# Optimization experiments

Measured on AMD Instinct MI355X. Metric: run time of the kernel, lower is better.

## Reference

```python
import jax, jax.numpy as jnp
import numpy as np

B, T, D, K, DEPTH = 8, 1024, 128, 64, 1


def _rel_ids(T, k):
    # relative_mat_id[i, j] = clamp(k + j - i, 0, 2k)
    base = jnp.arange(k, k + T)[None, :] - jnp.arange(T)[:, None]
    return jnp.clip(base, 0, 2 * k)  # [T, T] int32


def setup_inputs() -> dict:
    key = jax.random.key(0)
    ks = jax.random.split(key, 13)
    s = 1.0 / np.sqrt(D)
    return {
        "x": jax.random.normal(ks[0], (B, T, D), dtype=jnp.float32),
        "W0": jax.random.normal(ks[1], (D, D), dtype=jnp.float32) * s,
        "b0": jnp.zeros((D,), dtype=jnp.float32),
        "Wq": jax.random.normal(ks[2], (D, D), dtype=jnp.float32) * s,
        "bq": jnp.zeros((D,), dtype=jnp.float32),
        "Wk": jax.random.normal(ks[3], (D, D), dtype=jnp.float32) * s,
        "bk": jnp.zeros((D,), dtype=jnp.float32),
        "Wv": jax.random.normal(ks[4], (D, D), dtype=jnp.float32) * s,
        "bv": jnp.zeros((D,), dtype=jnp.float32),
        "W1": jax.random.normal(ks[5], (D, D), dtype=jnp.float32) * s,
        "b1": jnp.zeros((D,), dtype=jnp.float32),
        "pe_key": jax.random.normal(ks[6], (2 * K + 1, D), dtype=jnp.float32) * np.sqrt(2.0 / (2 * K + 1)),
        "pe_value": jax.random.normal(ks[7], (2 * K + 1, D), dtype=jnp.float32) * np.sqrt(2.0 / (2 * K + 1)),
    }


def reference(x, W0, b0, Wq, bq, Wk, bk, Wv, bv, W1, b1, pe_key, pe_value):
    Tlen = x.shape[1]
    ids = _rel_ids(Tlen, K)                     # [T, T]
    rpr_key = pe_key[ids]                       # [T, T, D]
    rpr_value = pe_value[ids]                   # [T, T, D]

    hs = jax.nn.relu(x @ W0 + b0)               # fc0 (dropout = eval identity)
    for _ in range(DEPTH):
        q = jnp.tanh(hs @ Wq + bq)
        k = jnp.tanh(hs @ Wk + bk)
        v = jnp.tanh(hs @ Wv + bv)
        a = jnp.einsum("bid,bjd->bij", q, k)
        a = a + jnp.einsum("ijd,bid->bij", rpr_key, q)
        a = jax.nn.softmax(a, axis=2)
        c = jnp.einsum("bij,bjd->bid", a, v)
        c = c + jnp.einsum("bij,ijd->bid", a, rpr_value)
        hs = jax.nn.relu(c @ W1 + b1)
    return hs
```

## Files before the change

kernel.cpp:

```cpp
#include <hip/hip_runtime.h>


#define TT 1024
#define DD 128
#define NB 8
#define SJH 1160

typedef _Float16 f16;
typedef __attribute__((ext_vector_type(8))) _Float16 f16x8;
typedef __attribute__((ext_vector_type(4))) _Float16 f16x4;
typedef __attribute__((ext_vector_type(4))) float f32x4;

static __device__ inline float fast_tanh(float x) {
    float xc = fminf(fmaxf(x, -12.f), 12.f);
    float e = __expf(2.f * xc);
    return (e - 1.f) / (e + 1.f);
}

#define GLDS(gp, lp) __builtin_amdgcn_global_load_lds( \
    (const __attribute__((address_space(1))) unsigned*)(gp), \
    (__attribute__((address_space(3))) unsigned*)(lp), 16, 0, 0)

__global__ __launch_bounds__(256) void prep_all(
        const float* __restrict__ W0, const float* __restrict__ Wq,
        const float* __restrict__ Wk, const float* __restrict__ Wv,
        const float* __restrict__ W1, const float* __restrict__ PEK,
        const float* __restrict__ PEV, char* __restrict__ wimg,
        char* __restrict__ pekimg, char* __restrict__ pevimg) {
    const int blk = blockIdx.x, t = threadIdx.x;
    if (blk < 5) {
        const float* W = blk == 0 ? W0 : blk == 1 ? Wq : blk == 2 ? Wk
                       : blk == 3 ? Wv : W1;
        char* o = wimg + (size_t)blk * 32768;
        #pragma unroll
        for (int it = 0; it < 8; it++) {
            int item = t + 256 * it;
            int n = item & 127, k0 = (item >> 7) * 8;
            f16x8 h;
            #pragma unroll
            for (int e = 0; e < 8; e++) h[e] = (f16)W[(k0 + e) * 128 + n];
            *(f16x8*)(o + n * 256 + ((2 * k0) ^ ((n & 7) << 4))) = h;
        }
    } else if (blk == 5) {
        for (int it = 0; it < 64; it++) {
            int idx = t + 256 * it;
            int m = idx >> 7, d = idx & 127;
            *(f16*)(pekimg + (m >> 6) * 16384 + (m & 63) * 256
                    + ((2 * d) ^ ((m & 7) << 4))) = (f16)PEK[m * 128 + d];
        }
    } else {
        for (int it = 0; it < 64; it++) {
            int idx = t + 256 * it;
            int m = idx >> 7, d = idx & 127;
            *(f16*)(pevimg + (m >> 5) * 8192 + d * 64
                    + ((2 * (m & 31)) ^ ((d & 3) << 4))) = (f16)PEV[m * 128 + d];
        }
    }
}

#define ZACC() do { _Pragma("unroll") for (int _i = 0; _i < 2; _i++) \
    _Pragma("unroll") for (int _j = 0; _j < 2; _j++) \
        acc[_i][_j] = (f32x4){0.f, 0.f, 0.f, 0.f}; } while (0)

#define GEMMCORE(SRC, WL) do { \
    _Pragma("unroll") for (int _c = 0; _c < 4; _c++) { \
        f16x8 _af[2], _bf[2]; \
        _Pragma("unroll") for (int _it = 0; _it < 2; _it++) { \
            int _row = _it * 16 + (l & 15); \
            int _a = (_row << 8) + (_c << 6) + ((l >> 4) << 4); \
            _af[_it] = *(const f16x8*)((SRC) + (_a ^ ((_row & 7) << 4))); } \
        _Pragma("unroll") for (int _nt = 0; _nt < 2; _nt++) { \
            int _n = wv * 32 + _nt * 16 + (l & 15); \
            int _a = (_n << 8) + (_c << 6) + ((l >> 4) << 4); \
            _bf[_nt] = *(const f16x8*)((WL) + (_a ^ ((_n & 7) << 4))); } \
        _Pragma("unroll") for (int _it = 0; _it < 2; _it++) \
        _Pragma("unroll") for (int _nt = 0; _nt < 2; _nt++) \
            acc[_it][_nt] = __builtin_amdgcn_mfma_f32_16x16x32_f16( \
                    _af[_it], _bf[_nt], acc[_it][_nt], 0, 0, 0); } } while (0)

#define ISSUEW(wi, dst) do { \
    const char* _g = wimg + (size_t)(wi) * 32768 + t * 16; \
    char* _d = (dst) + t * 16; \
    _Pragma("unroll") for (int _i = 0; _i < 8; _i++) \
        GLDS(_g + _i * 4096, _d + _i * 4096); \
} while (0)

#define WAITBAR(N) do { \
    asm volatile("s_waitcnt vmcnt(" #N ") lgkmcnt(0)" ::: "memory"); \
    __builtin_amdgcn_s_barrier(); \
    __builtin_amdgcn_sched_barrier(0); \
} while (0)

__global__ __launch_bounds__(256) void fused_qkv(
        const float* __restrict__ x, const char* __restrict__ wimg,
        const float* __restrict__ b0, const float* __restrict__ bq,
        const float* __restrict__ bk, const float* __restrict__ bv,
        f16* __restrict__ q16, char* __restrict__ kimg,
        char* __restrict__ vimg) {
    extern __shared__ __align__(16) char smq[];
    char* xs  = smq;
    char* hsl = smq + 8192;
    char* wA  = smq + 16384;
    char* wB  = smq + 49152;
    char* wC  = smq + 81920;
    const int t = threadIdx.x, wv = t >> 6, l = t & 63;
    const int blk = blockIdx.x;

    const int r0 = (blk & 7) * 1024 + (blk >> 3) * 32;
    ISSUEW(0, wA);
    ISSUEW(1, wB);
    {
        const float* X = x + (size_t)r0 * 128;
        #pragma unroll
        for (int i = 0; i < 2; i++) {
            f32x4 a0 = *(const f32x4*)(X + t * 16 + i * 8);
            f32x4 a1 = *(const f32x4*)(X + t * 16 + i * 8 + 4);
            f16x8 h;
            h[0]=(f16)a0[0]; h[1]=(f16)a0[1]; h[2]=(f16)a0[2]; h[3]=(f16)a0[3];
            h[4]=(f16)a1[0]; h[5]=(f16)a1[1]; h[6]=(f16)a1[2]; h[7]=(f16)a1[3];
            int a = t * 32 + i * 16;
            *(f16x8*)(xs + (a ^ (((a >> 8) & 7) << 4))) = h;
        }
    }
    WAITBAR(8);

    f32x4 acc[2][2];
    ZACC();
    GEMMCORE(xs, wA);
    {
        #pragma unroll
        for (int it = 0; it < 2; it++)
            #pragma unroll
            for (int nt = 0; nt < 2; nt++) {
                int n = wv * 32 + nt * 16 + (l & 15);
                float bb = b0[n];
                #pragma unroll
                for (int r = 0; r < 4; r++) {
                    int i = it * 16 + (l >> 4) * 4 + r;
                    float v = fmaxf(acc[it][nt][r] + bb, 0.f);
                    int a = i * 256 + 2 * n;
                    *(f16*)(hsl + (a ^ ((i & 7) << 4))) = (f16)v;
                }
            }
    }
    ISSUEW(2, wC);
    WAITBAR(8);

    ZACC();
    GEMMCORE(hsl, wB);
    {
        #pragma unroll
        for (int it = 0; it < 2; it++)
            #pragma unroll
            for (int nt = 0; nt < 2; nt++) {
                int n = wv * 32 + nt * 16 + (l & 15);
                float bb = bq[n];
                #pragma unroll
                for (int r = 0; r < 4; r++) {
                    int i = it * 16 + (l >> 4) * 4 + r;
                    q16[(size_t)(r0 + i) * 128 + n] =
                            (f16)fast_tanh(acc[it][nt][r] + bb);
                }
            }
    }
    ISSUEW(3, wA);
    WAITBAR(8);

    ZACC();
    GEMMCORE(hsl, wC);
    f16* ts = (f16*)xs;
    {
        #pragma unroll
        for (int it = 0; it < 2; it++)
            #pragma unroll
            for (int nt = 0; nt < 2; nt++) {
                int n = wv * 32 + nt * 16 + (l & 15);
                float bb = bk[n];
                #pragma unroll
                for (int r = 0; r < 4; r++) {
                    int i = it * 16 + (l >> 4) * 4 + r;
                    ts[i * 128 + n] = (f16)fast_tanh(acc[it][nt][r] + bb);
                }
            }
    }
    WAITBAR(0);

    {
        #pragma unroll
        for (int half = 0; half < 2; half++) {
            int row = (t >> 4) + half * 16;
            int seg = t & 15;
            int jg = r0 + row;
            int chunk = ((jg >> 10) << 4) + ((jg & 1023) >> 6);
            int jp = jg & 63;
            char* dst = kimg + (size_t)chunk * 16384 + jp * 256
                      + ((seg * 16) ^ ((jp & 7) << 4));
            *(f16x8*)dst = *(const f16x8*)&ts[row * 128 + seg * 8];
        }
    }
    ZACC();
    GEMMCORE(hsl, wA);
    {
        #pragma unroll
        for (int it = 0; it < 2; it++)
            #pragma unroll
            for (int nt = 0; nt < 2; nt++) {
                int d = wv * 32 + nt * 16 + (l & 15);
                float bb = bv[d];
                f16x4 h;
                #pragma unroll
                for (int r = 0; r < 4; r++)
                    h[r] = (f16)fast_tanh(acc[it][nt][r] + bb);
                int jb = r0 + it * 16 + ((l >> 4) << 2);
                int chunk = ((jb >> 10) << 5) + ((jb & 1023) >> 5);
                char* dst = vimg + (size_t)chunk * 8192 + d * 64
                          + ((2 * (jb & 31)) ^ ((d & 3) << 4));
                *(f16x4*)dst = h;
            }
    }
}

#define ISSUE16(src, bi) do { const char* _g = (src) + t * 16; \
    char* _d = BUF + (size_t)(bi) * 16384 + t * 16; \
    GLDS(_g, _d); GLDS(_g + 4096, _d + 4096); \
    GLDS(_g + 8192, _d + 8192); GLDS(_g + 12288, _d + 12288); \
} while (0)

#define ISSUE8(src, s8) do { const char* _g = (src) + t * 16; \
    char* _d = BUF + (size_t)(s8) * 8192 + t * 16; \
    GLDS(_g, _d); GLDS(_g + 4096, _d + 4096); \
} while (0)

__global__ __launch_bounds__(256) void attn_all(
        const f16* __restrict__ q16, const char* __restrict__ kimg,
        const char* __restrict__ pekimg, const char* __restrict__ vimg,
        const char* __restrict__ pevimg, const float* __restrict__ PEK,
        const float* __restrict__ PEV, const char* __restrict__ w1img,
        const float* __restrict__ b1, float* __restrict__ out) {
    extern __shared__ __align__(16) char sm7[];
    f16*   S   = (f16*)sm7;
    char*  BUF = sm7 + 37120;
    f16*   QB  = (f16*)(sm7 + 69888);
    float* LR  = (float*)(sm7 + 74112);

    const int t = threadIdx.x, wv = t >> 6, l = t & 63;
    const int lr = l & 15, lg = l >> 4;
    const int b = blockIdx.x & 7;
    const int i0 = (blockIdx.x >> 3) << 4;

    f16x8 qf[4];
    {
        const f16* qb = q16 + (size_t)(b * TT + i0 + lr) * 128 + lg * 8;
        #pragma unroll
        for (int c = 0; c < 4; c++) qf[c] = *(const f16x8*)(qb + c * 32);
    }
    const int row2 = t >> 4, l16 = t & 15;
    f16x8 qpv = *(const f16x8*)(q16 + (size_t)(b * TT + i0 + row2) * 128 + l16 * 8);
    f32x4 pkv0 = *(const f32x4*)(PEK + 128 * 128 + l16 * 8);
    f32x4 pkv1 = *(const f32x4*)(PEK + 128 * 128 + l16 * 8 + 4);
    f32x4 pvr4[2];
    #pragma unroll
    for (int dt = 0; dt < 2; dt++)
        pvr4[dt] = *(const f32x4*)(PEV + 128 * 128 + wv * 32 + dt * 16 + lg * 4);
    float bb1[2];
    #pragma unroll
    for (int nt = 0; nt < 2; nt++) bb1[nt] = b1[wv * 32 + nt * 16 + lr];

    const char* kbase = kimg + (size_t)b * 16 * 16384;
    const char* vbase = vimg + (size_t)b * 32 * 8192;

    ISSUE16(kbase, 0);

    for (int ch = 0; ch < 18; ch++) {
        asm volatile("s_waitcnt vmcnt(0)" ::: "memory");
        __builtin_amdgcn_s_barrier();
        __builtin_amdgcn_sched_barrier(0);
        {
            int ci = ch + 1;
            if (ci < 16)      ISSUE16(kbase + (size_t)ci * 16384, ci & 1);
            else if (ci < 18) ISSUE16(pekimg + (size_t)(ci - 16) * 16384, ci & 1);
            else {
                ISSUE8(vbase, 0);
                ISSUE8(vbase + 8192, 1);
            }
        }
        const char* kb = BUF + (size_t)(ch & 1) * 16384;
        const int jp = wv * 16 + lr;
        f32x4 a2 = {0.f, 0.f, 0.f, 0.f};
        #pragma unroll
        for (int c = 0; c < 4; c++) {
            f16x8 kf = *(const f16x8*)(kb + jp * 256
                        + ((c * 64 + lg * 16) ^ ((jp & 7) << 4)));
            a2 = __builtin_amdgcn_mfma_f32_16x16x32_f16(kf, qf[c], a2, 0, 0, 0);
        }
        f16x4 h = {(f16)a2[0], (f16)a2[1], (f16)a2[2], (f16)a2[3]};
        *(f16x4*)&S[lr * SJH + ch * 64 + wv * 16 + lg * 4] = h;
    }
    asm volatile("s_waitcnt lgkmcnt(0)" ::: "memory");
    __builtin_amdgcn_s_barrier();
    __builtin_amdgcn_sched_barrier(0);

    {
        const int ig = i0 + row2;
        f16* srow = S + row2 * SJH;
        f16* qrow = QB + row2 * 132;

        float qp;
        {
            float s = 0.f;
            #pragma unroll
            for (int e = 0; e < 4; e++) s += (float)qpv[e] * pkv0[e];
            #pragma unroll
            for (int e = 0; e < 4; e++) s += (float)qpv[e + 4] * pkv1[e];
            #pragma unroll
            for (int off = 8; off; off >>= 1) s += __shfl_xor(s, off, 64);
            qp = s;
        }
        for (int mm = l16; mm < 128; mm += 16) {
            qrow[mm] = srow[1024 + mm];
            srow[1024 + mm] = (f16)0.f;
        }
        if (l16 == 0) qrow[128] = (f16)qp;
        const float qlo = (float)qrow[0], qhi = qp;

        float lmax = -3.0e38f;
        #pragma unroll
        for (int kk = 0; kk < 8; kk++) {
            int j0 = kk * 128 + l16 * 8;
            f16x8 sv = *(const f16x8*)(srow + j0);
            #pragma unroll
            for (int e = 0; e < 8; e++) {
                int idd = 64 + j0 + e - ig;
                float qv = (idd <= 0) ? qlo : (idd >= 128 ? qhi : (float)qrow[idd]);
                lmax = fmaxf(lmax, (float)sv[e] + qv);
            }
        }
        #pragma unroll
        for (int off = 8; off; off >>= 1) lmax = fmaxf(lmax, __shfl_xor(lmax, off, 64));

        float lsum = 0.f, s0 = 0.f, s1 = 0.f;
        #pragma unroll
        for (int kk = 0; kk < 8; kk++) {
            int j0 = kk * 128 + l16 * 8;
            f16x8 sv = *(const f16x8*)(srow + j0);
            f16x8 pv;
            #pragma unroll
            for (int e = 0; e < 8; e++) {
                int idd = 64 + j0 + e - ig;
                float qv = (idd <= 0) ? qlo : (idd >= 128 ? qhi : (float)qrow[idd]);
                float p = __expf((float)sv[e] + qv - lmax);
                pv[e] = (f16)p;
                lsum += p;
                if (idd <= 0)        s0 += p;
                else if (idd >= 128) s1 += p;
                else                 srow[1024 + idd] = (f16)p;
            }
            *(f16x8*)(srow + j0) = pv;
        }
        #pragma unroll
        for (int off = 8; off; off >>= 1) {
            lsum += __shfl_xor(lsum, off, 64);
            s0   += __shfl_xor(s0,   off, 64);
            s1   += __shfl_xor(s1,   off, 64);
        }
        if (l16 == 0) {
            srow[1024] = (f16)s0;
            srow[1152] = (f16)s1;
            LR[row2] = lsum;
        }
    }
    asm volatile("s_waitcnt lgkmcnt(0)" ::: "memory");
    __builtin_amdgcn_s_barrier();
    __builtin_amdgcn_sched_barrier(0);
    ISSUE8(vbase + 2 * 8192, 2);

    f32x4 cacc[2] = {};
    for (int ch = 0; ch < 36; ch++) {
        asm volatile("s_waitcnt vmcnt(4)" ::: "memory");
        __builtin_amdgcn_s_barrier();
        __builtin_amdgcn_sched_barrier(0);
        {
            int ci = ch + 3;
            if (ci < 32)      ISSUE8(vbase + (size_t)ci * 8192, ci & 3);
            else if (ci < 36) ISSUE8(pevimg + (size_t)(ci - 32) * 8192, ci & 3);
            else              ISSUE8(w1img + (size_t)(ci - 36) * 8192, ci & 3);
        }
        const char* vb = BUF + (size_t)(ch & 3) * 8192;
        f16x8 pf = *(const f16x8*)&S[lr * SJH + ch * 32 + lg * 8];
        #pragma unroll
        for (int dt = 0; dt < 2; dt++) {
            int dp = wv * 32 + dt * 16 + lr;
            f16x8 vf = *(const f16x8*)(vb + dp * 64
                        + ((lg * 16) ^ ((dp & 3) << 4)));
            cacc[dt] = __builtin_amdgcn_mfma_f32_16x16x32_f16(vf, pf, cacc[dt], 0, 0, 0);
        }
    }

    const float w128 = (float)S[lr * SJH + 1152];
    const float rden = 1.f / LR[lr];
    asm volatile("s_waitcnt lgkmcnt(0)" ::: "memory");
    __builtin_amdgcn_s_barrier();
    __builtin_amdgcn_sched_barrier(0);
    ISSUE8(w1img + 3 * 8192, 3);
    char* cl = (char*)S;
    #pragma unroll
    for (int dt = 0; dt < 2; dt++) {
        #pragma unroll
        for (int r = 0; r < 4; r++) {
            int d = wv * 32 + dt * 16 + lg * 4 + r;
            float cv = (cacc[dt][r] + w128 * pvr4[dt][r]) * rden;
            int a = lr * 256 + 2 * d;
            *(f16*)(cl + (a ^ ((lr & 7) << 4))) = (f16)cv;
        }
    }
    asm volatile("s_waitcnt vmcnt(0) lgkmcnt(0)" ::: "memory");
    __builtin_amdgcn_s_barrier();
    __builtin_amdgcn_sched_barrier(0);

    const char* wl4 = BUF;
    f32x4 oacc[2] = {};
    #pragma unroll
    for (int c = 0; c < 4; c++) {
        int aa = lr * 256 + c * 64 + lg * 16;
        f16x8 af = *(const f16x8*)(cl + (aa ^ ((lr & 7) << 4)));
        #pragma unroll
        for (int nt = 0; nt < 2; nt++) {
            int n = wv * 32 + nt * 16 + lr;
            int ba = n * 256 + c * 64 + lg * 16;
            f16x8 bf = *(const f16x8*)(wl4 + (ba ^ ((n & 7) << 4)));
            oacc[nt] = __builtin_amdgcn_mfma_f32_16x16x32_f16(af, bf, oacc[nt], 0, 0, 0);
        }
    }
    #pragma unroll
    for (int nt = 0; nt < 2; nt++) {
        int n = wv * 32 + nt * 16 + lr;
        #pragma unroll
        for (int r = 0; r < 4; r++) {
            int i = lg * 4 + r;
            out[(size_t)(b * TT + i0 + i) * DD + n] = fmaxf(oacc[nt][r] + bb1[nt], 0.f);
        }
    }
}


extern "C" void kernel_launch(void* const* d_in, const int* in_sizes, int n_in,
                              void* d_out, int out_size, void* d_ws, size_t ws_size,
                              hipStream_t stream) {
    const float* x   = (const float*)d_in[0];
    const float* W0  = (const float*)d_in[1];
    const float* b0  = (const float*)d_in[2];
    const float* Wq  = (const float*)d_in[3];
    const float* bq  = (const float*)d_in[4];
    const float* Wk  = (const float*)d_in[5];
    const float* bk  = (const float*)d_in[6];
    const float* Wv  = (const float*)d_in[7];
    const float* bv  = (const float*)d_in[8];
    const float* W1  = (const float*)d_in[9];
    const float* b1  = (const float*)d_in[10];
    const float* pek = (const float*)d_in[11];
    const float* pev = (const float*)d_in[12];
    float* out = (float*)d_out;

    const size_t NTD = (size_t)NB * TT * DD;
    f16* q16     = (f16*)d_ws;
    char* wimg   = (char*)(q16 + NTD);
    char* kimg   = wimg + 5 * 32768;
    char* vimg   = kimg + (size_t)128 * 16384;
    char* pekimg = vimg + (size_t)256 * 8192;
    char* pevimg = pekimg + 32768;

    const int SMEM_QKV  = 114688;
    const int SMEM_ATTN = 74176;
    hipFuncSetAttribute(reinterpret_cast<const void*>(fused_qkv),
                        hipFuncAttributeMaxDynamicSharedMemorySize, SMEM_QKV);
    hipFuncSetAttribute(reinterpret_cast<const void*>(attn_all),
                        hipFuncAttributeMaxDynamicSharedMemorySize, SMEM_ATTN);

    hipLaunchKernelGGL(prep_all, dim3(7), dim3(256), 0, stream,
                       W0, Wq, Wk, Wv, W1, pek, pev, wimg, pekimg, pevimg);
    hipLaunchKernelGGL(fused_qkv, dim3(256), dim3(256), SMEM_QKV, stream,
                       x, wimg, b0, bq, bk, bv, q16, kimg, vimg);
    hipLaunchKernelGGL(attn_all, dim3(512), dim3(256), SMEM_ATTN, stream,
                       q16, kimg, pekimg, vimg, pevimg, pek, pev,
                       wimg + 4 * 32768, b1, out);
}
```

Measured before the change: 51.06 us.

## Split attention over key halves with a separate softmax combine kernel

Result: slower. 60.66 us (+18.8%).

```diff
diff --git a/kernel.cpp b/kernel.cpp
--- a/kernel.cpp
+++ b/kernel.cpp
@@ -4,7 +4,7 @@
 #define TT 1024
 #define DD 128
 #define NB 8
-#define SJH 1160
+#define SW 648
 
 typedef _Float16 f16;
 typedef __attribute__((ext_vector_type(8))) _Float16 f16x8;
@@ -26,7 +26,7 @@
         const float* __restrict__ Wk, const float* __restrict__ Wv,
         const float* __restrict__ W1, const float* __restrict__ PEK,
         const float* __restrict__ PEV, char* __restrict__ wimg,
-        char* __restrict__ pekimg, char* __restrict__ pevimg) {
+        char* __restrict__ pek4, char* __restrict__ pevt) {
     const int blk = blockIdx.x, t = threadIdx.x;
     if (blk < 5) {
         const float* W = blk == 0 ? W0 : blk == 1 ? Wq : blk == 2 ? Wk
@@ -45,15 +45,16 @@
         for (int it = 0; it < 64; it++) {
             int idx = t + 256 * it;
             int m = idx >> 7, d = idx & 127;
-            *(f16*)(pekimg + (m >> 6) * 16384 + (m & 63) * 256
-                    + ((2 * d) ^ ((m & 7) << 4))) = (f16)PEK[m * 128 + d];
+            int mp = m & 31;
+            *(f16*)(pek4 + (m >> 5) * 8192 + mp * 256
+                    + ((2 * d) ^ ((mp & 7) << 4))) = (f16)PEK[m * 128 + d];
         }
     } else {
         for (int it = 0; it < 64; it++) {
             int idx = t + 256 * it;
             int m = idx >> 7, d = idx & 127;
-            *(f16*)(pevimg + (m >> 5) * 8192 + d * 64
-                    + ((2 * (m & 31)) ^ ((d & 3) << 4))) = (f16)PEV[m * 128 + d];
+            *(f16*)(pevt + d * 256 + ((2 * m) ^ ((d & 7) << 4)))
+                    = (f16)PEV[m * 128 + d];
         }
     }
 }
@@ -191,9 +192,9 @@
             int row = (t >> 4) + half * 16;
             int seg = t & 15;
             int jg = r0 + row;
-            int chunk = ((jg >> 10) << 4) + ((jg & 1023) >> 6);
-            int jp = jg & 63;
-            char* dst = kimg + (size_t)chunk * 16384 + jp * 256
+            int chunk = ((jg >> 10) << 5) + ((jg & 1023) >> 5);
+            int jp = jg & 31;
+            char* dst = kimg + (size_t)chunk * 8192 + jp * 256
                       + ((seg * 16) ^ ((jp & 7) << 4));
             *(f16x8*)dst = *(const f16x8*)&ts[row * 128 + seg * 8];
         }
@@ -220,72 +221,77 @@
     }
 }
 
-#define ISSUE16(src, bi) do { const char* _g = (src) + t * 16; \
-    char* _d = BUF + (size_t)(bi) * 16384 + t * 16; \
-    GLDS(_g, _d); GLDS(_g + 4096, _d + 4096); \
-    GLDS(_g + 8192, _d + 8192); GLDS(_g + 12288, _d + 12288); \
-} while (0)
-
-#define ISSUE8(src, s8) do { const char* _g = (src) + t * 16; \
-    char* _d = BUF + (size_t)(s8) * 8192 + t * 16; \
+#define ISSUE8P(src, s8) do { const char* _g = (src) + t * 16; \
+    char* _d = RING + (size_t)(s8) * 8192 + t * 16; \
     GLDS(_g, _d); GLDS(_g + 4096, _d + 4096); \
 } while (0)
 
-__global__ __launch_bounds__(256) void attn_all(
+__global__ __launch_bounds__(256) void attn_part(
         const f16* __restrict__ q16, const char* __restrict__ kimg,
-        const char* __restrict__ pekimg, const char* __restrict__ vimg,
-        const char* __restrict__ pevimg, const float* __restrict__ PEK,
-        const float* __restrict__ PEV, const char* __restrict__ w1img,
-        const float* __restrict__ b1, float* __restrict__ out) {
-    extern __shared__ __align__(16) char sm7[];
-    f16*   S   = (f16*)sm7;
-    char*  BUF = sm7 + 37120;
-    f16*   QB  = (f16*)(sm7 + 69888);
-    float* LR  = (float*)(sm7 + 74112);
+        const char* __restrict__ pek4, const char* __restrict__ vimg,
+        const float* __restrict__ PEK, float* __restrict__ Cp,
+        float* __restrict__ Wp, float* __restrict__ MLp) {
+    extern __shared__ __align__(16) char smp[];
+    f16*   S    = (f16*)smp;
+    char*  RING = smp + 41472;
+    f16*   QB   = (f16*)(smp + 66048);
+    float* MLm  = (float*)(smp + 74496);
+    float* MLl  = (float*)(smp + 74624);
 
     const int t = threadIdx.x, wv = t >> 6, l = t & 63;
     const int lr = l & 15, lg = l >> 4;
-    const int b = blockIdx.x & 7;
-    const int i0 = (blockIdx.x >> 3) << 4;
+    const int blk = blockIdx.x;
+    const int b = blk & 7;
+    const int tile8 = blk >> 3;
+    const int itile = tile8 >> 1, h = tile8 & 1;
+    const int i0 = itile * 32;
+    const int ihalf16 = (wv & 1) << 4;
+    const int jsub16 = (wv >> 1) << 4;
 
     f16x8 qf[4];
     {
-        const f16* qb = q16 + (size_t)(b * TT + i0 + lr) * 128 + lg * 8;
+        const f16* qb = q16 + (size_t)(b * TT + i0 + ihalf16 + lr) * 128 + lg * 8;
         #pragma unroll
         for (int c = 0; c < 4; c++) qf[c] = *(const f16x8*)(qb + c * 32);
     }
-    const int row2 = t >> 4, l16 = t & 15;
-    f16x8 qpv = *(const f16x8*)(q16 + (size_t)(b * TT + i0 + row2) * 128 + l16 * 8);
-    f32x4 pkv0 = *(const f32x4*)(PEK + 128 * 128 + l16 * 8);
-    f32x4 pkv1 = *(const f32x4*)(PEK + 128 * 128 + l16 * 8 + 4);
-    f32x4 pvr4[2];
-    #pragma unroll
-    for (int dt = 0; dt < 2; dt++)
-        pvr4[dt] = *(const f32x4*)(PEV + 128 * 128 + wv * 32 + dt * 16 + lg * 4);
-    float bb1[2];
-    #pragma unroll
-    for (int nt = 0; nt < 2; nt++) bb1[nt] = b1[wv * 32 + nt * 16 + lr];
-
-    const char* kbase = kimg + (size_t)b * 16 * 16384;
-    const char* vbase = vimg + (size_t)b * 32 * 8192;
-
-    ISSUE16(kbase, 0);
-
-    for (int ch = 0; ch < 18; ch++) {
-        asm volatile("s_waitcnt vmcnt(0)" ::: "memory");
+    const int row = t >> 3, l8 = t & 7;
+    float qhi;
+    {
+        const f16* qr = q16 + (size_t)(b * TT + i0 + row) * 128 + l8 * 16;
+        f16x8 qa = *(const f16x8*)qr;
+        f16x8 qb2 = *(const f16x8*)(qr + 8);
+        const float* pr = PEK + 128 * 128 + l8 * 16;
+        float s = 0.f;
+        #pragma unroll
+        for (int e = 0; e < 8; e++) s += (float)qa[e] * pr[e];
+        #pragma unroll
+        for (int e = 0; e < 8; e++) s += (float)qb2[e] * pr[8 + e];
+        #pragma unroll
+        for (int off = 4; off; off >>= 1) s += __shfl_xor(s, off, 64);
+        qhi = s;
+    }
+    asm volatile("s_waitcnt vmcnt(0)" ::: "memory");
+    __builtin_amdgcn_sched_barrier(0);
+
+    const char* kbase = kimg + (size_t)(b * 32 + h * 16) * 8192;
+    const char* vbase = vimg + (size_t)(b * 32 + h * 16) * 8192;
+
+    ISSUE8P(kbase, 0);
+    ISSUE8P(kbase + 8192, 1);
+
+    for (int ch = 0; ch < 20; ch++) {
+        asm volatile("s_waitcnt vmcnt(2)" ::: "memory");
         __builtin_amdgcn_s_barrier();
         __builtin_amdgcn_sched_barrier(0);
         {
-            int ci = ch + 1;
-            if (ci < 16)      ISSUE16(kbase + (size_t)ci * 16384, ci & 1);
-            else if (ci < 18) ISSUE16(pekimg + (size_t)(ci - 16) * 16384, ci & 1);
-            else {
-                ISSUE8(vbase, 0);
-                ISSUE8(vbase + 8192, 1);
-            }
-        }
-        const char* kb = BUF + (size_t)(ch & 1) * 16384;
-        const int jp = wv * 16 + lr;
+            int ci = ch + 2;
+            const char* src = ci < 16 ? kbase + (size_t)ci * 8192
+                            : (ci < 20 ? pek4 + (size_t)(ci - 16) * 8192
+                                       : vbase + (size_t)(ci - 20) * 8192);
+            ISSUE8P(src, ci % 3);
+        }
+        const char* kb = RING + (size_t)(ch % 3) * 8192;
+        const int jp = jsub16 + lr;
         f32x4 a2 = {0.f, 0.f, 0.f, 0.f};
         #pragma unroll
         for (int c = 0; c < 4; c++) {
@@ -293,153 +299,258 @@
                         + ((c * 64 + lg * 16) ^ ((jp & 7) << 4)));
             a2 = __builtin_amdgcn_mfma_f32_16x16x32_f16(kf, qf[c], a2, 0, 0, 0);
         }
-        f16x4 h = {(f16)a2[0], (f16)a2[1], (f16)a2[2], (f16)a2[3]};
-        *(f16x4*)&S[lr * SJH + ch * 64 + wv * 16 + lg * 4] = h;
+        f16x4 hh = {(f16)a2[0], (f16)a2[1], (f16)a2[2], (f16)a2[3]};
+        if (ch < 16)
+            *(f16x4*)&S[(ihalf16 + lr) * SW + ch * 32 + jsub16 + lg * 4] = hh;
+        else
+            *(f16x4*)&QB[(ihalf16 + lr) * 132 + (ch - 16) * 32 + jsub16 + lg * 4] = hh;
     }
     asm volatile("s_waitcnt lgkmcnt(0)" ::: "memory");
     __builtin_amdgcn_s_barrier();
     __builtin_amdgcn_sched_barrier(0);
 
     {
-        const int ig = i0 + row2;
-        f16* srow = S + row2 * SJH;
-        f16* qrow = QB + row2 * 132;
-
-        float qp;
-        {
-            float s = 0.f;
-            #pragma unroll
-            for (int e = 0; e < 4; e++) s += (float)qpv[e] * pkv0[e];
-            #pragma unroll
-            for (int e = 0; e < 4; e++) s += (float)qpv[e + 4] * pkv1[e];
-            #pragma unroll
-            for (int off = 8; off; off >>= 1) s += __shfl_xor(s, off, 64);
-            qp = s;
-        }
-        for (int mm = l16; mm < 128; mm += 16) {
-            qrow[mm] = srow[1024 + mm];
-            srow[1024 + mm] = (f16)0.f;
-        }
-        if (l16 == 0) qrow[128] = (f16)qp;
-        const float qlo = (float)qrow[0], qhi = qp;
+        const int ig = i0 + row;
+        f16* srow = S + row * SW;
+        f16* qrow = QB + row * 132;
+        for (int m = l8; m < 132; m += 8) srow[512 + m] = (f16)0.f;
+        const float qlo = (float)qrow[0];
 
         float lmax = -3.0e38f;
         #pragma unroll
         for (int kk = 0; kk < 8; kk++) {
-            int j0 = kk * 128 + l16 * 8;
+            int j0 = kk * 64 + l8 * 8;
             f16x8 sv = *(const f16x8*)(srow + j0);
             #pragma unroll
             for (int e = 0; e < 8; e++) {
-                int idd = 64 + j0 + e - ig;
-                float qv = (idd <= 0) ? qlo : (idd >= 128 ? qhi : (float)qrow[idd]);
+                int idd = 64 + h * 512 + j0 + e - ig;
+                idd = idd < 0 ? 0 : (idd > 128 ? 128 : idd);
+                float qv = (idd == 0) ? qlo : (idd == 128 ? qhi : (float)qrow[idd]);
                 lmax = fmaxf(lmax, (float)sv[e] + qv);
             }
         }
         #pragma unroll
-        for (int off = 8; off; off >>= 1) lmax = fmaxf(lmax, __shfl_xor(lmax, off, 64));
+        for (int off = 4; off; off >>= 1) lmax = fmaxf(lmax, __shfl_xor(lmax, off, 64));
 
         float lsum = 0.f, s0 = 0.f, s1 = 0.f;
         #pragma unroll
         for (int kk = 0; kk < 8; kk++) {
-            int j0 = kk * 128 + l16 * 8;
+            int j0 = kk * 64 + l8 * 8;
             f16x8 sv = *(const f16x8*)(srow + j0);
             f16x8 pv;
             #pragma unroll
             for (int e = 0; e < 8; e++) {
-                int idd = 64 + j0 + e - ig;
-                float qv = (idd <= 0) ? qlo : (idd >= 128 ? qhi : (float)qrow[idd]);
+                int raw = 64 + h * 512 + j0 + e - ig;
+                int idd = raw < 0 ? 0 : (raw > 128 ? 128 : raw);
+                float qv = (idd == 0) ? qlo : (idd == 128 ? qhi : (float)qrow[idd]);
                 float p = __expf((float)sv[e] + qv - lmax);
                 pv[e] = (f16)p;
                 lsum += p;
-                if (idd <= 0)        s0 += p;
-                else if (idd >= 128) s1 += p;
-                else                 srow[1024 + idd] = (f16)p;
+                if (idd == 0)        s0 += p;
+                else if (idd == 128) s1 += p;
+                else                 srow[512 + idd] = (f16)p;
             }
             *(f16x8*)(srow + j0) = pv;
         }
         #pragma unroll
-        for (int off = 8; off; off >>= 1) {
+        for (int off = 4; off; off >>= 1) {
             lsum += __shfl_xor(lsum, off, 64);
             s0   += __shfl_xor(s0,   off, 64);
             s1   += __shfl_xor(s1,   off, 64);
         }
-        if (l16 == 0) {
-            srow[1024] = (f16)s0;
-            srow[1152] = (f16)s1;
-            LR[row2] = lsum;
+        if (l8 == 0) {
+            srow[512]       = (f16)s0;
+            srow[512 + 128] = (f16)s1;
+            MLm[row] = lmax;
+            MLl[row] = lsum;
         }
     }
     asm volatile("s_waitcnt lgkmcnt(0)" ::: "memory");
     __builtin_amdgcn_s_barrier();
     __builtin_amdgcn_sched_barrier(0);
-    ISSUE8(vbase + 2 * 8192, 2);
-
-    f32x4 cacc[2] = {};
-    for (int ch = 0; ch < 36; ch++) {
-        asm volatile("s_waitcnt vmcnt(4)" ::: "memory");
+
+    f32x4 cacc[2][2] = {};
+    for (int ch2 = 0; ch2 < 16; ch2++) {
+        const int g = 20 + ch2;
+        if (ch2 < 15) asm volatile("s_waitcnt vmcnt(2)" ::: "memory");
+        else          asm volatile("s_waitcnt vmcnt(0)" ::: "memory");
         __builtin_amdgcn_s_barrier();
         __builtin_amdgcn_sched_barrier(0);
-        {
-            int ci = ch + 3;
-            if (ci < 32)      ISSUE8(vbase + (size_t)ci * 8192, ci & 3);
-            else if (ci < 36) ISSUE8(pevimg + (size_t)(ci - 32) * 8192, ci & 3);
-            else              ISSUE8(w1img + (size_t)(ci - 36) * 8192, ci & 3);
-        }
-        const char* vb = BUF + (size_t)(ch & 3) * 8192;
-        f16x8 pf = *(const f16x8*)&S[lr * SJH + ch * 32 + lg * 8];
+        if (ch2 < 14)
+            ISSUE8P(vbase + (size_t)(ch2 + 2) * 8192, (g + 2) % 3);
+        const char* vb = RING + (size_t)(g % 3) * 8192;
+        #pragma unroll
+        for (int it2 = 0; it2 < 2; it2++) {
+            f16x8 pf = *(const f16x8*)&S[(it2 * 16 + lr) * SW + ch2 * 32 + lg * 8];
+            #pragma unroll
+            for (int dt = 0; dt < 2; dt++) {
+                int dp = wv * 32 + dt * 16 + lr;
+                f16x8 vf = *(const f16x8*)(vb + dp * 64
+                            + ((lg * 16) ^ ((dp & 3) << 4)));
+                cacc[dt][it2] = __builtin_amdgcn_mfma_f32_16x16x32_f16(
+                        vf, pf, cacc[dt][it2], 0, 0, 0);
+            }
+        }
+    }
+
+    #pragma unroll
+    for (int dt = 0; dt < 2; dt++)
+        #pragma unroll
+        for (int it2 = 0; it2 < 2; it2++) {
+            int i = it2 * 16 + lr;
+            int d0 = wv * 32 + dt * 16 + lg * 4;
+            *(f32x4*)&Cp[(size_t)blk * 4096 + i * 128 + d0] = cacc[dt][it2];
+        }
+    for (int m = l8; m < 129; m += 8)
+        Wp[(size_t)blk * 4224 + row * 132 + m] = (float)S[row * SW + 512 + m];
+    if (t < 32) {
+        MLp[(size_t)blk * 64 + t * 2]     = MLm[t];
+        MLp[(size_t)blk * 64 + t * 2 + 1] = MLl[t];
+    }
+}
+
+__global__ __launch_bounds__(256) void combine(
+        const float* __restrict__ Cp, const float* __restrict__ Wp,
+        const float* __restrict__ MLp, const char* __restrict__ pevt,
+        const char* __restrict__ w1img, const float* __restrict__ PEV,
+        const float* __restrict__ b1, float* __restrict__ out) {
+    extern __shared__ __align__(16) char smc[];
+    char*  PVl = smc;
+    char*  W1L = smc + 32768;
+    f16*   WC  = (f16*)(smc + 65536);
+    char*  CT  = smc + 74240;
+    float* RD  = (float*)(smc + 82432);
+    float* WH  = (float*)(smc + 82560);
+    float* A0  = (float*)(smc + 82688);
+    float* A1  = (float*)(smc + 82816);
+
+    const int t = threadIdx.x, wv = t >> 6, l = t & 63;
+    const int lr = l & 15, lg = l >> 4;
+    const int b = blockIdx.x & 7;
+    const int itile = blockIdx.x >> 3;
+    const int i0 = itile * 32;
+    const int p0 = b + 16 * itile, p1 = p0 + 8;
+
+    {
+        const char* g0 = pevt + t * 16;
+        const char* g1 = w1img + t * 16;
+        #pragma unroll
+        for (int i = 0; i < 8; i++) GLDS(g0 + i * 4096, PVl + t * 16 + i * 4096);
+        #pragma unroll
+        for (int i = 0; i < 8; i++) GLDS(g1 + i * 4096, W1L + t * 16 + i * 4096);
+    }
+    const int row = t >> 3, l8 = t & 7;
+    float m0 = MLp[(size_t)p0 * 64 + row * 2];
+    float l0 = MLp[(size_t)p0 * 64 + row * 2 + 1];
+    float m1 = MLp[(size_t)p1 * 64 + row * 2];
+    float l1 = MLp[(size_t)p1 * 64 + row * 2 + 1];
+    float mx = fmaxf(m0, m1);
+    float a0 = __expf(m0 - mx), a1 = __expf(m1 - mx);
+    if (l8 == 0) {
+        RD[row] = 1.f / (a0 * l0 + a1 * l1);
+        A0[row] = a0;
+        A1[row] = a1;
+    }
+    {
+        const float* w0r = Wp + (size_t)p0 * 4224 + row * 132;
+        const float* w1r = Wp + (size_t)p1 * 4224 + row * 132;
+        for (int m = l8; m < 129; m += 8) {
+            float mv = a0 * w0r[m] + a1 * w1r[m];
+            if (m < 128) WC[row * 136 + m] = (f16)mv;
+            else         WH[row] = mv;
+        }
+    }
+    float bb1[2];
+    f32x4 pvr4[2];
+    #pragma unroll
+    for (int nt = 0; nt < 2; nt++) bb1[nt] = b1[wv * 32 + nt * 16 + lr];
+    #pragma unroll
+    for (int dt = 0; dt < 2; dt++)
+        pvr4[dt] = *(const f32x4*)(PEV + 128 * 128 + wv * 32 + dt * 16 + lg * 4);
+
+    asm volatile("s_waitcnt vmcnt(0) lgkmcnt(0)" ::: "memory");
+    __builtin_amdgcn_s_barrier();
+    __builtin_amdgcn_sched_barrier(0);
+
+    f32x4 acc[2][2] = {};
+    #pragma unroll
+    for (int c = 0; c < 4; c++) {
+        f16x8 pvf[2], wf[2];
         #pragma unroll
         for (int dt = 0; dt < 2; dt++) {
             int dp = wv * 32 + dt * 16 + lr;
-            f16x8 vf = *(const f16x8*)(vb + dp * 64
-                        + ((lg * 16) ^ ((dp & 3) << 4)));
-            cacc[dt] = __builtin_amdgcn_mfma_f32_16x16x32_f16(vf, pf, cacc[dt], 0, 0, 0);
-        }
-    }
-
-    const float w128 = (float)S[lr * SJH + 1152];
-    const float rden = 1.f / LR[lr];
+            pvf[dt] = *(const f16x8*)(PVl + dp * 256
+                        + ((c * 64 + lg * 16) ^ ((dp & 7) << 4)));
+        }
+        #pragma unroll
+        for (int it2 = 0; it2 < 2; it2++)
+            wf[it2] = *(const f16x8*)((char*)WC + (it2 * 16 + lr) * 272
+                        + c * 64 + lg * 16);
+        #pragma unroll
+        for (int dt = 0; dt < 2; dt++)
+            #pragma unroll
+            for (int it2 = 0; it2 < 2; it2++)
+                acc[dt][it2] = __builtin_amdgcn_mfma_f32_16x16x32_f16(
+                        pvf[dt], wf[it2], acc[dt][it2], 0, 0, 0);
+    }
+
+    #pragma unroll
+    for (int dt = 0; dt < 2; dt++)
+        #pragma unroll
+        for (int it2 = 0; it2 < 2; it2++) {
+            int i = it2 * 16 + lr;
+            int d0 = wv * 32 + dt * 16 + lg * 4;
+            float a0i = A0[i], a1i = A1[i], rdi = RD[i], wh = WH[i];
+            f32x4 c0 = *(const f32x4*)&Cp[(size_t)p0 * 4096 + i * 128 + d0];
+            f32x4 c1 = *(const f32x4*)&Cp[(size_t)p1 * 4096 + i * 128 + d0];
+            #pragma unroll
+            for (int r = 0; r < 4; r++) {
+                int d = d0 + r;
+                float val = (acc[dt][it2][r] + a0i * c0[r] + a1i * c1[r]
+                             + wh * pvr4[dt][r]) * rdi;
+                int a = i * 256 + 2 * d;
+                *(f16*)(CT + (a ^ ((i & 7) << 4))) = (f16)val;
+            }
+        }
     asm volatile("s_waitcnt lgkmcnt(0)" ::: "memory");
     __builtin_amdgcn_s_barrier();
     __builtin_amdgcn_sched_barrier(0);
-    ISSUE8(w1img + 3 * 8192, 3);
-    char* cl = (char*)S;
-    #pragma unroll
-    for (int dt = 0; dt < 2; dt++) {
-        #pragma unroll
-        for (int r = 0; r < 4; r++) {
-            int d = wv * 32 + dt * 16 + lg * 4 + r;
-            float cv = (cacc[dt][r] + w128 * pvr4[dt][r]) * rden;
-            int a = lr * 256 + 2 * d;
-            *(f16*)(cl + (a ^ ((lr & 7) << 4))) = (f16)cv;
-        }
-    }
-    asm volatile("s_waitcnt vmcnt(0) lgkmcnt(0)" ::: "memory");
-    __builtin_amdgcn_s_barrier();
-    __builtin_amdgcn_sched_barrier(0);
-
-    const char* wl4 = BUF;
-    f32x4 oacc[2] = {};
+
+    f32x4 oacc[2][2] = {};
     #pragma unroll
     for (int c = 0; c < 4; c++) {
-        int aa = lr * 256 + c * 64 + lg * 16;
-        f16x8 af = *(const f16x8*)(cl + (aa ^ ((lr & 7) << 4)));
+        f16x8 af[2], bf[2];
+        #pragma unroll
+        for (int it2 = 0; it2 < 2; it2++) {
+            int ri = it2 * 16 + lr;
+            int aa = ri * 256 + c * 64 + lg * 16;
+            af[it2] = *(const f16x8*)(CT + (aa ^ ((ri & 7) << 4)));
+        }
         #pragma unroll
         for (int nt = 0; nt < 2; nt++) {
             int n = wv * 32 + nt * 16 + lr;
             int ba = n * 256 + c * 64 + lg * 16;
-            f16x8 bf = *(const f16x8*)(wl4 + (ba ^ ((n & 7) << 4)));
-            oacc[nt] = __builtin_amdgcn_mfma_f32_16x16x32_f16(af, bf, oacc[nt], 0, 0, 0);
-        }
+            bf[nt] = *(const f16x8*)(W1L + (ba ^ ((n & 7) << 4)));
+        }
+        #pragma unroll
+        for (int it2 = 0; it2 < 2; it2++)
+            #pragma unroll
+            for (int nt = 0; nt < 2; nt++)
+                oacc[it2][nt] = __builtin_amdgcn_mfma_f32_16x16x32_f16(
+                        af[it2], bf[nt], oacc[it2][nt], 0, 0, 0);
     }
     #pragma unroll
-    for (int nt = 0; nt < 2; nt++) {
-        int n = wv * 32 + nt * 16 + lr;
-        #pragma unroll
-        for (int r = 0; r < 4; r++) {
-            int i = lg * 4 + r;
-            out[(size_t)(b * TT + i0 + i) * DD + n] = fmaxf(oacc[nt][r] + bb1[nt], 0.f);
-        }
-    }
+    for (int it2 = 0; it2 < 2; it2++)
+        #pragma unroll
+        for (int nt = 0; nt < 2; nt++) {
+            int n = wv * 32 + nt * 16 + lr;
+            #pragma unroll
+            for (int r = 0; r < 4; r++) {
+                int i = it2 * 16 + lg * 4 + r;
+                out[(size_t)(b * TT + i0 + i) * DD + n]
+                        = fmaxf(oacc[it2][nt][r] + bb1[nt], 0.f);
+            }
+        }
 }
 
 
@@ -462,25 +573,32 @@
     float* out = (float*)d_out;
 
     const size_t NTD = (size_t)NB * TT * DD;
-    f16* q16     = (f16*)d_ws;
-    char* wimg   = (char*)(q16 + NTD);
-    char* kimg   = wimg + 5 * 32768;
-    char* vimg   = kimg + (size_t)128 * 16384;
-    char* pekimg = vimg + (size_t)256 * 8192;
-    char* pevimg = pekimg + 32768;
+    f16*  q16   = (f16*)d_ws;
+    char* wimg  = (char*)(q16 + NTD);
+    char* kimg  = wimg + 5 * 32768;
+    char* vimg  = kimg + (size_t)256 * 8192;
+    char* pek4  = vimg + (size_t)256 * 8192;
+    char* pevt  = pek4 + 32768;
+    float* Cp   = (float*)(pevt + 32768);
+    float* Wp   = Cp + (size_t)512 * 4096;
+    float* MLp  = Wp + (size_t)512 * 4224;
 
     const int SMEM_QKV  = 114688;
-    const int SMEM_ATTN = 74176;
+    const int SMEM_PART = 74752;
+    const int SMEM_COMB = 82944;
     hipFuncSetAttribute(reinterpret_cast<const void*>(fused_qkv),
                         hipFuncAttributeMaxDynamicSharedMemorySize, SMEM_QKV);
-    hipFuncSetAttribute(reinterpret_cast<const void*>(attn_all),
-                        hipFuncAttributeMaxDynamicSharedMemorySize, SMEM_ATTN);
+    hipFuncSetAttribute(reinterpret_cast<const void*>(attn_part),
+                        hipFuncAttributeMaxDynamicSharedMemorySize, SMEM_PART);
+    hipFuncSetAttribute(reinterpret_cast<const void*>(combine),
+                        hipFuncAttributeMaxDynamicSharedMemorySize, SMEM_COMB);
 
     hipLaunchKernelGGL(prep_all, dim3(7), dim3(256), 0, stream,
-                       W0, Wq, Wk, Wv, W1, pek, pev, wimg, pekimg, pevimg);
+                       W0, Wq, Wk, Wv, W1, pek, pev, wimg, pek4, pevt);
     hipLaunchKernelGGL(fused_qkv, dim3(256), dim3(256), SMEM_QKV, stream,
                        x, wimg, b0, bq, bk, bv, q16, kimg, vimg);
-    hipLaunchKernelGGL(attn_all, dim3(512), dim3(256), SMEM_ATTN, stream,
-                       q16, kimg, pekimg, vimg, pevimg, pek, pev,
-                       wimg + 4 * 32768, b1, out);
+    hipLaunchKernelGGL(attn_part, dim3(512), dim3(256), SMEM_PART, stream,
+                       q16, kimg, pek4, vimg, pek, Cp, Wp, MLp);
+    hipLaunchKernelGGL(combine, dim3(256), dim3(256), SMEM_COMB, stream,
+                       Cp, Wp, MLp, pevt, wimg + 4 * 32768, pev, b1, out);
 }
```
